# Performance work log

Hardware: AMD Instinct MI355X
Metric: run time of the kernel (lower is better)

Reference implementation:

```python
import jax, jax.numpy as jnp
import numpy as np

B, N, D, H, O, A, L = 128, 100, 2048, 1024, 1600, 400, 2048


def _mlp(x, w1, b1, w2, b2, w3, b3):
    h = jax.nn.relu(x @ w1 + b1)
    h = jax.nn.relu(h @ w2 + b2)
    return jax.nn.softmax(h @ w3 + b3, axis=2)  # softmax over class dim (dim=2)


def setup_inputs() -> dict:
    key = jax.random.key(0)
    ks = jax.random.split(key, 18)

    def lin(kw, fan_in, fan_out):
        s = 1.0 / np.sqrt(fan_in)
        return jax.random.normal(kw, (fan_in, fan_out), jnp.float32) * s

    x = jax.random.normal(ks[0], (B, N, D), jnp.float32)
    num_descs = jax.random.randint(ks[1], (B,), 0, N, jnp.int32)
    label_img = jnp.sort(jax.random.randint(ks[2], (L,), 0, B, jnp.int32))
    obj_labels = jax.random.randint(ks[3], (L,), 0, O)
    att_labels = jax.random.randint(ks[4], (L,), 0, A)

    inp = dict(x=x, num_descs=num_descs, label_img=label_img,
               obj_labels=obj_labels, att_labels=att_labels,
               w1o=lin(ks[5], D, H), b1o=jnp.zeros((H,), jnp.float32),
               w2o=lin(ks[6], H, H), b2o=jnp.zeros((H,), jnp.float32),
               w3o=lin(ks[7], H, O), b3o=jnp.zeros((O,), jnp.float32),
               w1a=lin(ks[8], D, H), b1a=jnp.zeros((H,), jnp.float32),
               w2a=lin(ks[9], H, H), b2a=jnp.zeros((H,), jnp.float32),
               w3a=lin(ks[10], H, A), b3a=jnp.zeros((A,), jnp.float32))
    return inp


def reference(x, num_descs, label_img, obj_labels, att_labels,
              w1o, b1o, w2o, b2o, w3o, b3o,
              w1a, b1a, w2a, b2a, w3a, b3a):
    po = _mlp(x, w1o, b1o, w2o, b2o, w3o, b3o)  # [B, N, O]
    pa = _mlp(x, w1a, b1a, w2a, b2a, w3a, b3a)  # [B, N, A]

    rows = jnp.arange(po.shape[1])  # [N]
    # per-label gather of the prob column for its object/attribute class -> [L, N]
    p_obj = po[label_img[:, None], rows[None, :], obj_labels[:, None]]
    p_att = pa[label_img[:, None], rows[None, :], att_labels[:, None]]
    # ragged unpad (descs beyond num_descs[img] excluded from argmax)
    valid = rows[None, :] < num_descs[label_img][:, None]
    score = jnp.where(valid, p_obj * p_att, -jnp.inf)
    desc = jnp.argmax(score, axis=1)  # [L]

    obj_dists = po[label_img, desc, :]  # [L, O]
    att_dists = pa[label_img, desc, :]  # [L, A]
    return (obj_dists, att_dists)
```

## Files before the change

kernel.cpp:

```cpp
#include <hip/hip_runtime.h>
#include <hip/hip_bf16.h>
#include <math.h>

#define Bq 128
#define Nq 100
#define Dq 2048
#define Hq 1024
#define Oq 1600
#define Aq 400
#define Lq 2048
#define Mq (Bq * Nq)
#define OqP 1664
#define AqP 512

typedef __attribute__((ext_vector_type(8))) short bf16x8;
typedef __attribute__((ext_vector_type(16))) float f32x16;
typedef unsigned short ushort;


__device__ __forceinline__ void split1(float v, ushort& h, ushort& l) {
    __hip_bfloat16 bh = __float2bfloat16(v);
    float fh = __bfloat162float(bh);
    __hip_bfloat16 bl = __float2bfloat16(v - fh);
    h = __builtin_bit_cast(ushort, bh);
    l = __builtin_bit_cast(ushort, bl);
}

__device__ __forceinline__ void gl_lds16(const ushort* g, ushort* lds) {
    __builtin_amdgcn_global_load_lds(
        (const __attribute__((address_space(1))) unsigned int*)g,
        (__attribute__((address_space(3))) unsigned int*)lds,
        16, 0, 0);
}

__global__ void build_offsets(const int* __restrict__ num_descs,
                              int* __restrict__ off, int* __restrict__ mc,
                              int* __restrict__ rowmap)
{
    __shared__ int cnt[Bq];
    __shared__ int offs[Bq + 1];
    const int t = threadIdx.x;
    int nd = num_descs[t];
    nd = nd < 0 ? 0 : (nd > Nq ? Nq : nd);
    const int c = nd < 1 ? 1 : nd;
    cnt[t] = c;
    __syncthreads();
    if (t == 0) {
        int s = 0;
        for (int i = 0; i < Bq; i++) { offs[i] = s; s += cnt[i]; }
        offs[Bq] = s;
        mc[0] = s;
        mc[1] = (s + 127) & ~127;
    }
    __syncthreads();
    off[t] = offs[t];
    for (int i = t; i < Mq; i += Bq) rowmap[i] = -1;
    __syncthreads();
    const int o = offs[t];
    for (int n = 0; n < c; n++) rowmap[o + n] = t * Nq + n;
}

__global__ void split_compact(const float* __restrict__ x,
                              const int* __restrict__ rowmap,
                              const int* __restrict__ mc,
                              ushort* __restrict__ hi, ushort* __restrict__ lo)
{
    const int KB = Dq / 16;
    const int wid = (blockIdx.x * blockDim.x + threadIdx.x) >> 6;
    const int lane = threadIdx.x & 63;
    const int rt = wid / KB;
    const int kb = wid - rt * KB;
    if (rt * 32 >= mc[1]) return;
    const int crow = rt * 32 + (lane & 31);
    const int k = kb * 16 + (lane >> 5) * 8;
    const int orig = (crow < mc[0]) ? rowmap[crow] : -1;
    ushort h[8], l[8];
    if (orig < 0) {
#pragma unroll
        for (int j = 0; j < 8; j++) { h[j] = 0; l[j] = 0; }
    } else {
        const float* src = x + (size_t)orig * Dq + k;
        float4 v0 = *(const float4*)(src);
        float4 v1 = *(const float4*)(src + 4);
        float v[8] = {v0.x, v0.y, v0.z, v0.w, v1.x, v1.y, v1.z, v1.w};
#pragma unroll
        for (int j = 0; j < 8; j++) split1(v[j], h[j], l[j]);
    }
    const size_t a = (size_t)wid * 512 + (size_t)lane * 8;
    *(bf16x8*)(hi + a) = *(bf16x8*)h;
    *(bf16x8*)(lo + a) = *(bf16x8*)l;
}

struct TSeg { const float* W; ushort* Th; ushort* Tl; int K; int N; int gx; int base; };
struct TSegs { TSeg s[6]; };

__global__ void tsplit_all(TSegs a)
{
    const int id = blockIdx.x;
    TSeg sg = a.s[5];
#pragma unroll
    for (int i = 4; i >= 0; i--) if (id < a.s[i + 1].base) sg = a.s[i];
    const int local = id - sg.base;
    const int bn = (local % sg.gx) * 32;
    const int bk = (local / sg.gx) * 32;
    const int KB = sg.K >> 4;

    __shared__ float t[32][33];
    const int tx = threadIdx.x & 31, ty = threadIdx.x >> 5;
#pragma unroll
    for (int i = 0; i < 4; i++) {
        const int k = bk + ty + i * 8, n = bn + tx;
        t[ty + i * 8][tx] = (n < sg.N) ? sg.W[(size_t)k * sg.N + n] : 0.f;
    }
    __syncthreads();

    const int wave = threadIdx.x >> 6;
    const int lane = threadIdx.x & 63;
    const int kc = wave & 1;
    const int hl = wave >> 1;
    const int nloc = lane & 31;
    const int kloc = kc * 16 + (lane >> 5) * 8;
    ushort v8[8];
#pragma unroll
    for (int e = 0; e < 8; e++) {
        ushort h, l;
        split1(t[kloc + e][nloc], h, l);
        v8[e] = hl ? l : h;
    }
    const size_t chunk = (size_t)((bn >> 5)) * KB + (bk >> 4) + kc;
    ushort* dst = (hl ? sg.Tl : sg.Th) + chunk * 512 + (size_t)lane * 8;
    *(bf16x8*)dst = *(bf16x8*)v8;
}

struct GArgs {
    const ushort* Ah; const ushort* Al;
    const ushort* Bh; const ushort* Bl;
    const float* bias;
    float* Cf; ushort* Ch; ushort* Cl;
    int K, Npad, Nreal, ldc, mode;
};

__global__ __launch_bounds__(256, 2) void gemm_split(GArgs g0, GArgs g1,
                                                     const int* __restrict__ mcp)
{
    const GArgs g = (blockIdx.z == 0) ? g0 : g1;
    const int bm = blockIdx.y * 128;
    const int bn = blockIdx.x * 128;
    if (bn >= g.Npad) return;
    if (bm >= mcp[1]) return;

    const int KB = g.K >> 4;

    __shared__ __align__(16) ushort sAh[8192];
    __shared__ __align__(16) ushort sAl[8192];
    __shared__ __align__(16) ushort sBh[8192];
    __shared__ __align__(16) ushort sBl[8192];

    const int tid  = threadIdx.x;
    const int wave = tid >> 6;
    const int lane = tid & 63;
    const int wmi = (wave >> 1) * 2;
    const int wni = (wave & 1) * 2;
    const int l31  = lane & 31;
    const int half = lane >> 5;

    const ushort* gAh = g.Ah + ((size_t)(bm / 32 + wave) * KB) * 512 + lane * 8;
    const ushort* gAl = g.Al + ((size_t)(bm / 32 + wave) * KB) * 512 + lane * 8;
    const ushort* gBh = g.Bh + ((size_t)(bn / 32 + wave) * KB) * 512 + lane * 8;
    const ushort* gBl = g.Bl + ((size_t)(bn / 32 + wave) * KB) * 512 + lane * 8;

    f32x16 acc[2][2] = {};

    auto STAGE = [&](int c) {
        const size_t go = (size_t)c * 512;
        const int ls = ((c & 3) << 11) + (wave << 9);
        gl_lds16(gAh + go, &sAh[ls]);
        gl_lds16(gAl + go, &sAl[ls]);
        gl_lds16(gBh + go, &sBh[ls]);
        gl_lds16(gBl + go, &sBl[ls]);
    };

    auto PHASE = [&](int c, int stage_c, int drain) {
        const int slot = (c & 3) << 11;
        bf16x8 ah[2], al[2], bh[2], bl[2];
#pragma unroll
        for (int i = 0; i < 2; i++) {
            const int sa = slot + (wmi + i) * 512 + lane * 8;
            const int sb = slot + (wni + i) * 512 + lane * 8;
            ah[i] = *(const bf16x8*)&sAh[sa];
            al[i] = *(const bf16x8*)&sAl[sa];
            bh[i] = *(const bf16x8*)&sBh[sb];
            bl[i] = *(const bf16x8*)&sBl[sb];
        }
        if (stage_c >= 0) STAGE(stage_c);
        asm volatile("s_waitcnt lgkmcnt(0)" ::: "memory");
        __builtin_amdgcn_sched_barrier(0);
        __builtin_amdgcn_s_setprio(1);
#pragma unroll
        for (int i = 0; i < 2; i++)
#pragma unroll
            for (int j = 0; j < 2; j++) {
                acc[i][j] = __builtin_amdgcn_mfma_f32_32x32x16_bf16(ah[i], bh[j], acc[i][j], 0, 0, 0);
                acc[i][j] = __builtin_amdgcn_mfma_f32_32x32x16_bf16(ah[i], bl[j], acc[i][j], 0, 0, 0);
                acc[i][j] = __builtin_amdgcn_mfma_f32_32x32x16_bf16(al[i], bh[j], acc[i][j], 0, 0, 0);
            }
        __builtin_amdgcn_s_setprio(0);
        __builtin_amdgcn_sched_barrier(0);
        if (drain == 8)      asm volatile("s_waitcnt vmcnt(8)" ::: "memory");
        else if (drain == 4) asm volatile("s_waitcnt vmcnt(4)" ::: "memory");
        else if (drain == 0) asm volatile("s_waitcnt vmcnt(0)" ::: "memory");
        if (drain >= 0)      asm volatile("s_barrier" ::: "memory");
    };

    STAGE(0); STAGE(1); STAGE(2);
    asm volatile("s_waitcnt vmcnt(8)" ::: "memory");
    asm volatile("s_barrier" ::: "memory");

    for (int c = 0; c < KB - 3; ++c) PHASE(c, c + 3, 8);
    PHASE(KB - 3, -1, 4);
    PHASE(KB - 2, -1, 0);
    PHASE(KB - 1, -1, -1);

    const int KC = g.ldc >> 4;
#pragma unroll
    for (int j = 0; j < 2; j++) {
        const int col = bn + (wni + j) * 32 + l31;
        if (col < g.Nreal) {
            const float bv = g.bias[col];
#pragma unroll
            for (int i = 0; i < 2; i++) {
#pragma unroll
                for (int r = 0; r < 16; r++) {
                    const int row = bm + (wmi + i) * 32 + (r & 3) + 8 * (r >> 2) + 4 * half;
                    float v = acc[i][j][r] + bv;
                    if (g.mode == 1) {
                        v = fmaxf(v, 0.f);
                        ushort h, l;
                        split1(v, h, l);
                        const size_t chunk = (size_t)(row >> 5) * KC + (col >> 4);
                        const size_t adr = chunk * 512
                            + (size_t)((row & 31) + 32 * ((col >> 3) & 1)) * 8 + (col & 7);
                        g.Ch[adr] = h;
                        g.Cl[adr] = l;
                    } else {
                        g.Cf[(size_t)row * g.ldc + col] = v;
                    }
                }
            }
        }
    }
}

__global__ void softmax_stats2(const float* __restrict__ Zo, const float* __restrict__ Za,
                               const int* __restrict__ mc,
                               float* __restrict__ mxo, float* __restrict__ smo,
                               float* __restrict__ mxa, float* __restrict__ sma)
{
    const int r = blockIdx.x;
    if (r >= mc[0]) return;
    const float* Z; int ncols; float* mx; float* sm;
    if (blockIdx.y == 0) { Z = Zo; ncols = Oq; mx = mxo; sm = smo; }
    else                 { Z = Za; ncols = Aq; mx = mxa; sm = sma; }
    const float* row = Z + (size_t)r * ncols;
    __shared__ float red[256];
    float m = -INFINITY;
    for (int c = threadIdx.x; c < ncols; c += 256) m = fmaxf(m, row[c]);
    red[threadIdx.x] = m;
    __syncthreads();
    for (int s = 128; s > 0; s >>= 1) {
        if (threadIdx.x < s) red[threadIdx.x] = fmaxf(red[threadIdx.x], red[threadIdx.x + s]);
        __syncthreads();
    }
    m = red[0];
    __syncthreads();
    float su = 0.f;
    for (int c = threadIdx.x; c < ncols; c += 256) su += expf(row[c] - m);
    red[threadIdx.x] = su;
    __syncthreads();
    for (int s = 128; s > 0; s >>= 1) {
        if (threadIdx.x < s) red[threadIdx.x] += red[threadIdx.x + s];
        __syncthreads();
    }
    if (threadIdx.x == 0) { mx[r] = m; sm[r] = red[0]; }
}

__global__ void argmax_gather(
    const float* __restrict__ Zo, const float* __restrict__ Za,
    const float* __restrict__ mxo, const float* __restrict__ smo,
    const float* __restrict__ mxa, const float* __restrict__ sma,
    const int* __restrict__ label_img, const int* __restrict__ num_descs,
    const int* __restrict__ obj_labels, const int* __restrict__ att_labels,
    const int* __restrict__ off, float* __restrict__ out)
{
    const int l = blockIdx.x;
    const int b = label_img[l];
    const int nd = num_descs[b];
    const int r0 = off[b];
    const int t = threadIdx.x;

    __shared__ float ss[128];
    __shared__ int   si[128];
    if (t < 128) {
        float score = -INFINITY;
        if (t < Nq && t < nd) {
            const int r = r0 + t;
            const float po = expf(Zo[(size_t)r * Oq + obj_labels[l]] - mxo[r]) / smo[r];
            const float pa = expf(Za[(size_t)r * Aq + att_labels[l]] - mxa[r]) / sma[r];
            score = po * pa;
        }
        ss[t] = score;
        si[t] = t;
    }
    __syncthreads();
    for (int s = 64; s > 0; s >>= 1) {
        if (t < s) {
            const float s2 = ss[t + s];
            const int   i2 = si[t + s];
            if (s2 > ss[t] || (s2 == ss[t] && i2 < si[t])) { ss[t] = s2; si[t] = i2; }
        }
        __syncthreads();
    }
    const int r = r0 + si[0];

    const float mo = mxo[r], so = smo[r];
    const float* zo = Zo + (size_t)r * Oq;
    float* oo = out + (size_t)l * Oq;
    for (int c = t; c < Oq; c += 256)
        oo[c] = expf(zo[c] - mo) / so;

    const float ma = mxa[r], sa = sma[r];
    const float* za = Za + (size_t)r * Aq;
    float* oa = out + (size_t)Lq * Oq + (size_t)l * Aq;
    for (int c = t; c < Aq; c += 256)
        oa[c] = expf(za[c] - ma) / sa;
}

extern "C" void kernel_launch(void* const* d_in, const int* in_sizes, int n_in,
                              void* d_out, int out_size, void* d_ws, size_t ws_size,
                              hipStream_t stream)
{
    const float* x          = (const float*)d_in[0];
    const int*   num_descs  = (const int*)d_in[1];
    const int*   label_img  = (const int*)d_in[2];
    const int*   obj_labels = (const int*)d_in[3];
    const int*   att_labels = (const int*)d_in[4];
    const float* w1o = (const float*)d_in[5];  const float* b1o = (const float*)d_in[6];
    const float* w2o = (const float*)d_in[7];  const float* b2o = (const float*)d_in[8];
    const float* w3o = (const float*)d_in[9];  const float* b3o = (const float*)d_in[10];
    const float* w1a = (const float*)d_in[11]; const float* b1a = (const float*)d_in[12];
    const float* w2a = (const float*)d_in[13]; const float* b2a = (const float*)d_in[14];
    const float* w3a = (const float*)d_in[15]; const float* b3a = (const float*)d_in[16];
    float* out = (float*)d_out;

    char* p = (char*)d_ws;
    auto carve = [&](size_t bytes) { char* q = p; p += (bytes + 255) & ~(size_t)255; return q; };

    char* bufA = carve((size_t)Mq * Dq * 2 * 2);
    char* bufB = carve((size_t)Mq * Hq * 2 * 2 * 2);
    ushort* w1oth = (ushort*)carve((size_t)Hq * Dq * 2);  ushort* w1otl = (ushort*)carve((size_t)Hq * Dq * 2);
    ushort* w1ath = (ushort*)carve((size_t)Hq * Dq * 2);  ushort* w1atl = (ushort*)carve((size_t)Hq * Dq * 2);
    ushort* w2oth = (ushort*)carve((size_t)Hq * Hq * 2);  ushort* w2otl = (ushort*)carve((size_t)Hq * Hq * 2);
    ushort* w2ath = (ushort*)carve((size_t)Hq * Hq * 2);  ushort* w2atl = (ushort*)carve((size_t)Hq * Hq * 2);
    ushort* w3oth = (ushort*)carve((size_t)OqP * Hq * 2); ushort* w3otl = (ushort*)carve((size_t)OqP * Hq * 2);
    ushort* w3ath = (ushort*)carve((size_t)AqP * Hq * 2); ushort* w3atl = (ushort*)carve((size_t)AqP * Hq * 2);
    float* mxo = (float*)carve(Mq * 4); float* smo = (float*)carve(Mq * 4);
    float* mxa = (float*)carve(Mq * 4); float* sma = (float*)carve(Mq * 4);
    int* off    = (int*)carve(Bq * 4);
    int* mc     = (int*)carve(2 * 4);
    int* rowmap = (int*)carve(Mq * 4);

    ushort* xh = (ushort*)bufA;
    ushort* xl = xh + (size_t)Mq * Dq;
    ushort* h2oh = (ushort*)bufA;
    ushort* h2ol = h2oh + (size_t)Mq * Hq;
    ushort* h2ah = h2ol + (size_t)Mq * Hq;
    ushort* h2al = h2ah + (size_t)Mq * Hq;
    ushort* h1oh = (ushort*)bufB;
    ushort* h1ol = h1oh + (size_t)Mq * Hq;
    ushort* h1ah = h1ol + (size_t)Mq * Hq;
    ushort* h1al = h1ah + (size_t)Mq * Hq;
    float* z3o = (float*)bufB;
    float* z3a = z3o + (size_t)Mq * Oq;

    build_offsets<<<1, 128, 0, stream>>>(num_descs, off, mc, rowmap);
    split_compact<<<(Mq / 32) * (Dq / 16) / 4, 256, 0, stream>>>(x, rowmap, mc, xh, xl);

    {
        TSegs ts;
        int base = 0;
        auto seg = [&](const float* W, ushort* Th, ushort* Tl, int K, int N, int Npad) {
            TSeg s; s.W = W; s.Th = Th; s.Tl = Tl; s.K = K; s.N = N;
            s.gx = Npad / 32; s.base = base; base += (Npad / 32) * (K / 32); return s;
        };
        ts.s[0] = seg(w1o, w1oth, w1otl, Dq, Hq, Hq);
        ts.s[1] = seg(w1a, w1ath, w1atl, Dq, Hq, Hq);
        ts.s[2] = seg(w2o, w2oth, w2otl, Hq, Hq, Hq);
        ts.s[3] = seg(w2a, w2ath, w2atl, Hq, Hq, Hq);
        ts.s[4] = seg(w3o, w3oth, w3otl, Hq, Oq, OqP);
        ts.s[5] = seg(w3a, w3ath, w3atl, Hq, Aq, AqP);
        tsplit_all<<<base, 256, 0, stream>>>(ts);
    }

    {
        GArgs go = { xh, xl, w1oth, w1otl, b1o, nullptr, h1oh, h1ol, Dq, Hq, Hq, Hq, 1 };
        GArgs ga = { xh, xl, w1ath, w1atl, b1a, nullptr, h1ah, h1al, Dq, Hq, Hq, Hq, 1 };
        gemm_split<<<dim3(Hq / 128, Mq / 128, 2), 256, 0, stream>>>(go, ga, mc);
    }
    {
        GArgs go = { h1oh, h1ol, w2oth, w2otl, b2o, nullptr, h2oh, h2ol, Hq, Hq, Hq, Hq, 1 };
        GArgs ga = { h1ah, h1al, w2ath, w2atl, b2a, nullptr, h2ah, h2al, Hq, Hq, Hq, Hq, 1 };
        gemm_split<<<dim3(Hq / 128, Mq / 128, 2), 256, 0, stream>>>(go, ga, mc);
    }
    {
        GArgs go = { h2oh, h2ol, w3oth, w3otl, b3o, z3o, nullptr, nullptr, Hq, OqP, Oq, Oq, 0 };
        GArgs ga = { h2ah, h2al, w3ath, w3atl, b3a, z3a, nullptr, nullptr, Hq, AqP, Aq, Aq, 0 };
        gemm_split<<<dim3(OqP / 128, Mq / 128, 2), 256, 0, stream>>>(go, ga, mc);
    }

    softmax_stats2<<<dim3(Mq, 2), 256, 0, stream>>>(z3o, z3a, mc, mxo, smo, mxa, sma);
    argmax_gather<<<Lq, 256, 0, stream>>>(z3o, z3a, mxo, smo, mxa, sma,
                                          label_img, num_descs, obj_labels, att_labels, off, out);
}
```

Before: 600.1 us.

## Enlarge GEMM tiles to 256x256 with 8 waves and XCD-aware block remapping

Doubles the GEMM block tile from 128x128 to 256x256 using 512 threads (8 waves), each wave computing a 128x64 sub-tile with 4x2 MFMA accumulators, and pads the object output width to 1792. It also flattens the grid into 1D, computing the active block count on device from the valid row count and remapping block indices so contiguous logical tiles land on the same XCD. The larger tiles raise arithmetic intensity and operand reuse per LDS load. In exchange they use 128KB of LDS and more registers per block, which may limit occupancy, and they give coarser tail handling for the ragged M dimension and the 400-wide attribute head.

Measured after the change: 645.6 us. 1.08x slower.

```diff
diff --git a/kernel.cpp b/kernel.cpp
--- a/kernel.cpp
+++ b/kernel.cpp
@@ -10,7 +10,7 @@
 #define Aq 400
 #define Lq 2048
 #define Mq (Bq * Nq)
-#define OqP 1664
+#define OqP 1792
 #define AqP 512
 
 typedef __attribute__((ext_vector_type(8))) short bf16x8;
@@ -140,27 +140,37 @@
     int K, Npad, Nreal, ldc, mode;
 };
 
-__global__ __launch_bounds__(256, 2) void gemm_split(GArgs g0, GArgs g1,
-                                                     const int* __restrict__ mcp)
-{
-    const GArgs g = (blockIdx.z == 0) ? g0 : g1;
-    const int bm = blockIdx.y * 128;
-    const int bn = blockIdx.x * 128;
+__global__ __launch_bounds__(512, 2) void gemm_split(GArgs g0, GArgs g1,
+                                                     const int* __restrict__ mcp,
+                                                     int gx)
+{
+    const int ny = (mcp[1] + 255) >> 8;
+    const int nact = gx * 2 * ny;
+    const int hw = blockIdx.x;
+    if (hw >= nact) return;
+    const int q = nact >> 3, r = nact & 7, xcd = hw & 7, pos = hw >> 3;
+    const int L = (xcd < r ? xcd * (q + 1) : r * (q + 1) + (xcd - r) * q) + pos;
+    const int bx = L % gx;
+    const int z  = (L / gx) & 1;
+    const int by = L / (gx * 2);
+
+    const GArgs g = z ? g1 : g0;
+    const int bm = by * 256;
+    const int bn = bx * 256;
     if (bn >= g.Npad) return;
-    if (bm >= mcp[1]) return;
 
     const int KB = g.K >> 4;
 
-    __shared__ __align__(16) ushort sAh[8192];
-    __shared__ __align__(16) ushort sAl[8192];
-    __shared__ __align__(16) ushort sBh[8192];
-    __shared__ __align__(16) ushort sBl[8192];
+    __shared__ __align__(16) ushort sAh[16384];
+    __shared__ __align__(16) ushort sAl[16384];
+    __shared__ __align__(16) ushort sBh[16384];
+    __shared__ __align__(16) ushort sBl[16384];
 
     const int tid  = threadIdx.x;
     const int wave = tid >> 6;
     const int lane = tid & 63;
-    const int wmi = (wave >> 1) * 2;
-    const int wni = (wave & 1) * 2;
+    const int wm = wave >> 2;
+    const int wn = wave & 3;
     const int l31  = lane & 31;
     const int half = lane >> 5;
 
@@ -169,11 +179,11 @@
     const ushort* gBh = g.Bh + ((size_t)(bn / 32 + wave) * KB) * 512 + lane * 8;
     const ushort* gBl = g.Bl + ((size_t)(bn / 32 + wave) * KB) * 512 + lane * 8;
 
-    f32x16 acc[2][2] = {};
+    f32x16 acc[4][2] = {};
 
     auto STAGE = [&](int c) {
         const size_t go = (size_t)c * 512;
-        const int ls = ((c & 3) << 11) + (wave << 9);
+        const int ls = ((c & 3) << 12) + (wave << 9);
         gl_lds16(gAh + go, &sAh[ls]);
         gl_lds16(gAl + go, &sAl[ls]);
         gl_lds16(gBh + go, &sBh[ls]);
@@ -181,23 +191,26 @@
     };
 
     auto PHASE = [&](int c, int stage_c, int drain) {
-        const int slot = (c & 3) << 11;
-        bf16x8 ah[2], al[2], bh[2], bl[2];
-#pragma unroll
-        for (int i = 0; i < 2; i++) {
-            const int sa = slot + (wmi + i) * 512 + lane * 8;
-            const int sb = slot + (wni + i) * 512 + lane * 8;
+        const int slot = (c & 3) << 12;
+        bf16x8 ah[4], al[4], bh[2], bl[2];
+#pragma unroll
+        for (int i = 0; i < 4; i++) {
+            const int sa = slot + (wm * 4 + i) * 512 + lane * 8;
             ah[i] = *(const bf16x8*)&sAh[sa];
             al[i] = *(const bf16x8*)&sAl[sa];
-            bh[i] = *(const bf16x8*)&sBh[sb];
-            bl[i] = *(const bf16x8*)&sBl[sb];
+        }
+#pragma unroll
+        for (int j = 0; j < 2; j++) {
+            const int sb = slot + (wn * 2 + j) * 512 + lane * 8;
+            bh[j] = *(const bf16x8*)&sBh[sb];
+            bl[j] = *(const bf16x8*)&sBl[sb];
         }
         if (stage_c >= 0) STAGE(stage_c);
         asm volatile("s_waitcnt lgkmcnt(0)" ::: "memory");
         __builtin_amdgcn_sched_barrier(0);
         __builtin_amdgcn_s_setprio(1);
 #pragma unroll
-        for (int i = 0; i < 2; i++)
+        for (int i = 0; i < 4; i++)
 #pragma unroll
             for (int j = 0; j < 2; j++) {
                 acc[i][j] = __builtin_amdgcn_mfma_f32_32x32x16_bf16(ah[i], bh[j], acc[i][j], 0, 0, 0);
@@ -224,14 +237,14 @@
     const int KC = g.ldc >> 4;
 #pragma unroll
     for (int j = 0; j < 2; j++) {
-        const int col = bn + (wni + j) * 32 + l31;
+        const int col = bn + (wn * 2 + j) * 32 + l31;
         if (col < g.Nreal) {
             const float bv = g.bias[col];
 #pragma unroll
-            for (int i = 0; i < 2; i++) {
+            for (int i = 0; i < 4; i++) {
 #pragma unroll
                 for (int r = 0; r < 16; r++) {
-                    const int row = bm + (wmi + i) * 32 + (r & 3) + 8 * (r >> 2) + 4 * half;
+                    const int row = bm + (wm * 4 + i) * 32 + (r & 3) + 8 * (r >> 2) + 4 * half;
                     float v = acc[i][j][r] + bv;
                     if (g.mode == 1) {
                         v = fmaxf(v, 0.f);
@@ -404,17 +417,17 @@
     {
         GArgs go = { xh, xl, w1oth, w1otl, b1o, nullptr, h1oh, h1ol, Dq, Hq, Hq, Hq, 1 };
         GArgs ga = { xh, xl, w1ath, w1atl, b1a, nullptr, h1ah, h1al, Dq, Hq, Hq, Hq, 1 };
-        gemm_split<<<dim3(Hq / 128, Mq / 128, 2), 256, 0, stream>>>(go, ga, mc);
+        gemm_split<<<(Hq / 256) * 2 * (Mq / 256), 512, 0, stream>>>(go, ga, mc, Hq / 256);
     }
     {
         GArgs go = { h1oh, h1ol, w2oth, w2otl, b2o, nullptr, h2oh, h2ol, Hq, Hq, Hq, Hq, 1 };
         GArgs ga = { h1ah, h1al, w2ath, w2atl, b2a, nullptr, h2ah, h2al, Hq, Hq, Hq, Hq, 1 };
-        gemm_split<<<dim3(Hq / 128, Mq / 128, 2), 256, 0, stream>>>(go, ga, mc);
+        gemm_split<<<(Hq / 256) * 2 * (Mq / 256), 512, 0, stream>>>(go, ga, mc, Hq / 256);
     }
     {
         GArgs go = { h2oh, h2ol, w3oth, w3otl, b3o, z3o, nullptr, nullptr, Hq, OqP, Oq, Oq, 0 };
         GArgs ga = { h2ah, h2al, w3ath, w3atl, b3a, z3a, nullptr, nullptr, Hq, AqP, Aq, Aq, 0 };
-        gemm_split<<<dim3(OqP / 128, Mq / 128, 2), 256, 0, stream>>>(go, ga, mc);
+        gemm_split<<<(OqP / 256) * 2 * (Mq / 256), 512, 0, stream>>>(go, ga, mc, OqP / 256);
     }
 
     softmax_stats2<<<dim3(Mq, 2), 256, 0, stream>>>(z3o, z3a, mc, mxo, smo, mxa, sma);
```

## Use 256x128 GEMM tiles with 8 waves, XCD-aware block remap, 3-stage LDS

Applied to the files above, without the earlier changes.

The split-bf16 GEMM now uses 512-thread blocks computing 256x128 tiles, so each B tile loaded into LDS is shared by twice as many rows. Launch becomes a 1D grid sized from the compacted row count, remapped so consecutive logical tiles land on the same XCD for L2 locality, and the o/a halves are merged into one tile index space. The LDS pipeline drops from 4 to 3 slots with adjusted vmcnt waits, and row padding goes to 256. This trades higher LDS use per block and more padded rows for better reuse and fewer wasted blocks.

Measured after the change: 593.1 us. About the same (-1.2%).

```diff
diff --git a/kernel.cpp b/kernel.cpp
--- a/kernel.cpp
+++ b/kernel.cpp
@@ -51,6 +51,7 @@
         offs[Bq] = s;
         mc[0] = s;
         mc[1] = (s + 127) & ~127;
+        mc[2] = (s + 255) & ~(int)255;
     }
     __syncthreads();
     off[t] = offs[t];
@@ -70,7 +71,7 @@
     const int lane = threadIdx.x & 63;
     const int rt = wid / KB;
     const int kb = wid - rt * KB;
-    if (rt * 32 >= mc[1]) return;
+    if (rt * 32 >= mc[2]) return;
     const int crow = rt * 32 + (lane & 31);
     const int k = kb * 16 + (lane >> 5) * 8;
     const int orig = (crow < mc[0]) ? rowmap[crow] : -1;
@@ -140,57 +141,65 @@
     int K, Npad, Nreal, ldc, mode;
 };
 
-__global__ __launch_bounds__(256, 2) void gemm_split(GArgs g0, GArgs g1,
-                                                     const int* __restrict__ mcp)
-{
-    const GArgs g = (blockIdx.z == 0) ? g0 : g1;
-    const int bm = blockIdx.y * 128;
-    const int bn = blockIdx.x * 128;
-    if (bn >= g.Npad) return;
-    if (bm >= mcp[1]) return;
+__global__ __launch_bounds__(512, 4) void gemm_split(GArgs g0, GArgs g1,
+                                                     const int* __restrict__ mcp,
+                                                     int nct0, int nct)
+{
+    const int ny = mcp[2] >> 8;
+    const int nact = nct * ny;
+    const int hw = blockIdx.x;
+    if (hw >= nact) return;
+    const int q = nact >> 3, r = nact & 7, xcd = hw & 7, pos = hw >> 3;
+    const int L = (xcd < r ? xcd * (q + 1) : r * (q + 1) + (xcd - r) * q) + pos;
+    const int by = L / nct;
+    const int ct = L - by * nct;
+
+    const GArgs g = (ct < nct0) ? g0 : g1;
+    const int bm = by * 256;
+    const int bn = (ct < nct0 ? ct : ct - nct0) * 128;
 
     const int KB = g.K >> 4;
 
-    __shared__ __align__(16) ushort sAh[8192];
-    __shared__ __align__(16) ushort sAl[8192];
-    __shared__ __align__(16) ushort sBh[8192];
-    __shared__ __align__(16) ushort sBl[8192];
+    __shared__ __align__(16) ushort S[36864];
 
     const int tid  = threadIdx.x;
     const int wave = tid >> 6;
     const int lane = tid & 63;
-    const int wmi = (wave >> 1) * 2;
-    const int wni = (wave & 1) * 2;
+    const int wm = wave >> 1;
+    const int wn = wave & 1;
     const int l31  = lane & 31;
     const int half = lane >> 5;
 
     const ushort* gAh = g.Ah + ((size_t)(bm / 32 + wave) * KB) * 512 + lane * 8;
     const ushort* gAl = g.Al + ((size_t)(bm / 32 + wave) * KB) * 512 + lane * 8;
-    const ushort* gBh = g.Bh + ((size_t)(bn / 32 + wave) * KB) * 512 + lane * 8;
-    const ushort* gBl = g.Bl + ((size_t)(bn / 32 + wave) * KB) * 512 + lane * 8;
+    const ushort* gB  = (wave < 4 ? g.Bh : g.Bl)
+                        + ((size_t)(bn / 32 + (wave & 3)) * KB) * 512 + lane * 8;
+    const int bOff = 8192 + (wave >= 4 ? 2048 : 0) + ((wave & 3) << 9);
 
     f32x16 acc[2][2] = {};
 
     auto STAGE = [&](int c) {
         const size_t go = (size_t)c * 512;
-        const int ls = ((c & 3) << 11) + (wave << 9);
-        gl_lds16(gAh + go, &sAh[ls]);
-        gl_lds16(gAl + go, &sAl[ls]);
-        gl_lds16(gBh + go, &sBh[ls]);
-        gl_lds16(gBl + go, &sBl[ls]);
+        const int slot = (c % 3) * 12288;
+        gl_lds16(gAh + go, &S[slot + (wave << 9)]);
+        gl_lds16(gAl + go, &S[slot + 4096 + (wave << 9)]);
+        gl_lds16(gB + go, &S[slot + bOff]);
     };
 
     auto PHASE = [&](int c, int stage_c, int drain) {
-        const int slot = (c & 3) << 11;
+        const int slot = (c % 3) * 12288;
         bf16x8 ah[2], al[2], bh[2], bl[2];
 #pragma unroll
         for (int i = 0; i < 2; i++) {
-            const int sa = slot + (wmi + i) * 512 + lane * 8;
-            const int sb = slot + (wni + i) * 512 + lane * 8;
-            ah[i] = *(const bf16x8*)&sAh[sa];
-            al[i] = *(const bf16x8*)&sAl[sa];
-            bh[i] = *(const bf16x8*)&sBh[sb];
-            bl[i] = *(const bf16x8*)&sBl[sb];
+            const int sa = slot + (wm * 2 + i) * 512 + lane * 8;
+            ah[i] = *(const bf16x8*)&S[sa];
+            al[i] = *(const bf16x8*)&S[sa + 4096];
+        }
+#pragma unroll
+        for (int j = 0; j < 2; j++) {
+            const int sb = slot + 8192 + (wn * 2 + j) * 512 + lane * 8;
+            bh[j] = *(const bf16x8*)&S[sb];
+            bl[j] = *(const bf16x8*)&S[sb + 2048];
         }
         if (stage_c >= 0) STAGE(stage_c);
         asm volatile("s_waitcnt lgkmcnt(0)" ::: "memory");
@@ -206,32 +215,30 @@
             }
         __builtin_amdgcn_s_setprio(0);
         __builtin_amdgcn_sched_barrier(0);
-        if (drain == 8)      asm volatile("s_waitcnt vmcnt(8)" ::: "memory");
-        else if (drain == 4) asm volatile("s_waitcnt vmcnt(4)" ::: "memory");
+        if (drain == 3)      asm volatile("s_waitcnt vmcnt(3)" ::: "memory");
         else if (drain == 0) asm volatile("s_waitcnt vmcnt(0)" ::: "memory");
         if (drain >= 0)      asm volatile("s_barrier" ::: "memory");
     };
 
-    STAGE(0); STAGE(1); STAGE(2);
-    asm volatile("s_waitcnt vmcnt(8)" ::: "memory");
+    STAGE(0); STAGE(1);
+    asm volatile("s_waitcnt vmcnt(3)" ::: "memory");
     asm volatile("s_barrier" ::: "memory");
 
-    for (int c = 0; c < KB - 3; ++c) PHASE(c, c + 3, 8);
-    PHASE(KB - 3, -1, 4);
+    for (int c = 0; c < KB - 2; ++c) PHASE(c, c + 2, 3);
     PHASE(KB - 2, -1, 0);
     PHASE(KB - 1, -1, -1);
 
     const int KC = g.ldc >> 4;
 #pragma unroll
     for (int j = 0; j < 2; j++) {
-        const int col = bn + (wni + j) * 32 + l31;
+        const int col = bn + (wn * 2 + j) * 32 + l31;
         if (col < g.Nreal) {
             const float bv = g.bias[col];
 #pragma unroll
             for (int i = 0; i < 2; i++) {
 #pragma unroll
                 for (int r = 0; r < 16; r++) {
-                    const int row = bm + (wmi + i) * 32 + (r & 3) + 8 * (r >> 2) + 4 * half;
+                    const int row = bm + (wm * 2 + i) * 32 + (r & 3) + 8 * (r >> 2) + 4 * half;
                     float v = acc[i][j][r] + bv;
                     if (g.mode == 1) {
                         v = fmaxf(v, 0.f);
@@ -366,7 +373,7 @@
     float* mxo = (float*)carve(Mq * 4); float* smo = (float*)carve(Mq * 4);
     float* mxa = (float*)carve(Mq * 4); float* sma = (float*)carve(Mq * 4);
     int* off    = (int*)carve(Bq * 4);
-    int* mc     = (int*)carve(2 * 4);
+    int* mc     = (int*)carve(4 * 4);
     int* rowmap = (int*)carve(Mq * 4);
 
     ushort* xh = (ushort*)bufA;
@@ -404,17 +411,19 @@
     {
         GArgs go = { xh, xl, w1oth, w1otl, b1o, nullptr, h1oh, h1ol, Dq, Hq, Hq, Hq, 1 };
         GArgs ga = { xh, xl, w1ath, w1atl, b1a, nullptr, h1ah, h1al, Dq, Hq, Hq, Hq, 1 };
-        gemm_split<<<dim3(Hq / 128, Mq / 128, 2), 256, 0, stream>>>(go, ga, mc);
+        gemm_split<<<16 * (Mq / 256), 512, 0, stream>>>(go, ga, mc, 8, 16);
     }
     {
         GArgs go = { h1oh, h1ol, w2oth, w2otl, b2o, nullptr, h2oh, h2ol, Hq, Hq, Hq, Hq, 1 };
         GArgs ga = { h1ah, h1al, w2ath, w2atl, b2a, nullptr, h2ah, h2al, Hq, Hq, Hq, Hq, 1 };
-        gemm_split<<<dim3(Hq / 128, Mq / 128, 2), 256, 0, stream>>>(go, ga, mc);
+        gemm_split<<<16 * (Mq / 256), 512, 0, stream>>>(go, ga, mc, 8, 16);
     }
     {
         GArgs go = { h2oh, h2ol, w3oth, w3otl, b3o, z3o, nullptr, nullptr, Hq, OqP, Oq, Oq, 0 };
         GArgs ga = { h2ah, h2al, w3ath, w3atl, b3a, z3a, nullptr, nullptr, Hq, AqP, Aq, Aq, 0 };
-        gemm_split<<<dim3(OqP / 128, Mq / 128, 2), 256, 0, stream>>>(go, ga, mc);
+        gemm_split<<<(OqP / 128 + AqP / 128) * (Mq / 256), 512, 0, stream>>>(go, ga, mc,
+                                                                            OqP / 128,
+                                                                            OqP / 128 + AqP / 128);
     }
 
     softmax_stats2<<<dim3(Mq, 2), 256, 0, stream>>>(z3o, z3a, mc, mxo, smo, mxa, sma);
```

## Flatten GEMM grid with XCD-aware tile remap and relax LDS wait placement

Applied to the files above, without the earlier changes.

Replaces the 3D grid with a 1D grid over only the active tiles, combining both MLP branches into one column range. Each hardware block id is mapped so consecutive logical tiles land on the same XCD, which should improve L2 reuse of A rows and B columns, and the third-layer launch no longer spawns idle blocks for the narrower attribute branch. It also moves the LDS wait from before the MFMAs to just before the barrier and removes the sched barriers, letting the compiler interleave LDS reads with MFMAs. The workspace slot for mc is enlarged, although the new path still reads only mc[1].

Result: faster. 578.0 us (-3.7%).

```diff
diff --git a/kernel.cpp b/kernel.cpp
--- a/kernel.cpp
+++ b/kernel.cpp
@@ -141,13 +141,21 @@
 };
 
 __global__ __launch_bounds__(256, 2) void gemm_split(GArgs g0, GArgs g1,
-                                                     const int* __restrict__ mcp)
-{
-    const GArgs g = (blockIdx.z == 0) ? g0 : g1;
-    const int bm = blockIdx.y * 128;
-    const int bn = blockIdx.x * 128;
-    if (bn >= g.Npad) return;
-    if (bm >= mcp[1]) return;
+                                                     const int* __restrict__ mcp,
+                                                     int nct0, int nct)
+{
+    const int ny = mcp[1] >> 7;
+    const int nact = nct * ny;
+    const int hw = blockIdx.x;
+    if (hw >= nact) return;
+    const int q = nact >> 3, r = nact & 7, xcd = hw & 7, pos = hw >> 3;
+    const int L = (xcd < r ? xcd * (q + 1) : r * (q + 1) + (xcd - r) * q) + pos;
+    const int by = L / nct;
+    const int ct = L - by * nct;
+
+    const GArgs g = (ct < nct0) ? g0 : g1;
+    const int bm = by * 128;
+    const int bn = (ct < nct0 ? ct : ct - nct0) * 128;
 
     const int KB = g.K >> 4;
 
@@ -193,8 +201,6 @@
             bl[i] = *(const bf16x8*)&sBl[sb];
         }
         if (stage_c >= 0) STAGE(stage_c);
-        asm volatile("s_waitcnt lgkmcnt(0)" ::: "memory");
-        __builtin_amdgcn_sched_barrier(0);
         __builtin_amdgcn_s_setprio(1);
 #pragma unroll
         for (int i = 0; i < 2; i++)
@@ -205,11 +211,13 @@
                 acc[i][j] = __builtin_amdgcn_mfma_f32_32x32x16_bf16(al[i], bh[j], acc[i][j], 0, 0, 0);
             }
         __builtin_amdgcn_s_setprio(0);
-        __builtin_amdgcn_sched_barrier(0);
         if (drain == 8)      asm volatile("s_waitcnt vmcnt(8)" ::: "memory");
         else if (drain == 4) asm volatile("s_waitcnt vmcnt(4)" ::: "memory");
         else if (drain == 0) asm volatile("s_waitcnt vmcnt(0)" ::: "memory");
-        if (drain >= 0)      asm volatile("s_barrier" ::: "memory");
+        if (drain >= 0) {
+            asm volatile("s_waitcnt lgkmcnt(0)" ::: "memory");
+            asm volatile("s_barrier" ::: "memory");
+        }
     };
 
     STAGE(0); STAGE(1); STAGE(2);
@@ -366,7 +374,7 @@
     float* mxo = (float*)carve(Mq * 4); float* smo = (float*)carve(Mq * 4);
     float* mxa = (float*)carve(Mq * 4); float* sma = (float*)carve(Mq * 4);
     int* off    = (int*)carve(Bq * 4);
-    int* mc     = (int*)carve(2 * 4);
+    int* mc     = (int*)carve(4 * 4);
     int* rowmap = (int*)carve(Mq * 4);
 
     ushort* xh = (ushort*)bufA;
@@ -404,17 +412,19 @@
     {
         GArgs go = { xh, xl, w1oth, w1otl, b1o, nullptr, h1oh, h1ol, Dq, Hq, Hq, Hq, 1 };
         GArgs ga = { xh, xl, w1ath, w1atl, b1a, nullptr, h1ah, h1al, Dq, Hq, Hq, Hq, 1 };
-        gemm_split<<<dim3(Hq / 128, Mq / 128, 2), 256, 0, stream>>>(go, ga, mc);
+        gemm_split<<<16 * (Mq / 128), 256, 0, stream>>>(go, ga, mc, 8, 16);
     }
     {
         GArgs go = { h1oh, h1ol, w2oth, w2otl, b2o, nullptr, h2oh, h2ol, Hq, Hq, Hq, Hq, 1 };
         GArgs ga = { h1ah, h1al, w2ath, w2atl, b2a, nullptr, h2ah, h2al, Hq, Hq, Hq, Hq, 1 };
-        gemm_split<<<dim3(Hq / 128, Mq / 128, 2), 256, 0, stream>>>(go, ga, mc);
+        gemm_split<<<16 * (Mq / 128), 256, 0, stream>>>(go, ga, mc, 8, 16);
     }
     {
         GArgs go = { h2oh, h2ol, w3oth, w3otl, b3o, z3o, nullptr, nullptr, Hq, OqP, Oq, Oq, 0 };
         GArgs ga = { h2ah, h2al, w3ath, w3atl, b3a, z3a, nullptr, nullptr, Hq, AqP, Aq, Aq, 0 };
-        gemm_split<<<dim3(OqP / 128, Mq / 128, 2), 256, 0, stream>>>(go, ga, mc);
+        gemm_split<<<(OqP / 128 + AqP / 128) * (Mq / 128), 256, 0, stream>>>(go, ga, mc,
+                                                                            OqP / 128,
+                                                                            OqP / 128 + AqP / 128);
     }
 
     softmax_stats2<<<dim3(Mq, 2), 256, 0, stream>>>(z3o, z3a, mc, mxo, smo, mxa, sma);
```
